# Kernel optimization log

Hardware: AMD Instinct MI355X
Metric: run time of the kernel (lower is better)

The kernel has to match this reference:

```python
import jax, jax.numpy as jnp
import numpy as np

N_HEADS, D_MODEL, D_HEAD = 16, 1024, 64
INIT_STD = 0.02


def setup_inputs() -> dict:
    key = jax.random.key(0)
    ks = jax.random.split(key, 5)
    x = jax.random.normal(ks[0], (4, 2048, D_MODEL), dtype=jnp.float32)
    W_Q = jax.random.normal(ks[1], (N_HEADS, D_MODEL, D_HEAD), dtype=jnp.float32) * INIT_STD
    W_K = jax.random.normal(ks[2], (N_HEADS, D_MODEL, D_HEAD), dtype=jnp.float32) * INIT_STD
    W_V = jax.random.normal(ks[3], (N_HEADS, D_MODEL, D_HEAD), dtype=jnp.float32) * INIT_STD
    W_O = jax.random.normal(ks[4], (N_HEADS, D_HEAD, D_MODEL), dtype=jnp.float32) * INIT_STD
    b_Q = jnp.zeros((N_HEADS, D_HEAD), dtype=jnp.float32)
    b_K = jnp.zeros((N_HEADS, D_HEAD), dtype=jnp.float32)
    b_V = jnp.zeros((N_HEADS, D_HEAD), dtype=jnp.float32)
    b_O = jnp.zeros((D_MODEL,), dtype=jnp.float32)
    return {"normalized_resid_pre": x, "W_Q": W_Q, "W_K": W_K, "W_V": W_V,
            "W_O": W_O, "b_Q": b_Q, "b_K": b_K, "b_V": b_V, "b_O": b_O}


def reference(normalized_resid_pre, W_Q, W_K, W_V, W_O, b_Q, b_K, b_V, b_O):
    x = normalized_resid_pre  # [b, s, d_model]
    q = jnp.einsum('bsm,hmd->bshd', x, W_Q) + b_Q  # [b, s, h, d_head]
    k = jnp.einsum('bsm,hmd->bshd', x, W_K) + b_K
    v = jnp.einsum('bsm,hmd->bshd', x, W_V) + b_V
    scores = jnp.einsum('bqhd,bkhd->bhqk', q, k) / jnp.sqrt(jnp.float32(D_HEAD))
    S = x.shape[1]
    causal = jnp.tril(jnp.ones((S, S), dtype=bool))  # keep key_pos <= query_pos
    scores = jnp.where(causal, scores, jnp.finfo(scores.dtype).min)
    pattern = jax.nn.softmax(scores, axis=-1)  # [b, h, q, k]
    z = jnp.einsum('bhqk,bkhd->bqhd', pattern, v)
    attn_out = jnp.einsum('bqhd,hdm->bqm', z, W_O) + b_O
    return attn_out
```

## Files before the change

kernel.cpp:

```cpp
#include <hip/hip_runtime.h>
#include <hip/hip_bf16.h>
#include <math.h>

typedef __bf16 bf16_t;
typedef bf16_t bf16x8 __attribute__((ext_vector_type(8)));
typedef float f32x4 __attribute__((ext_vector_type(4)));

#define BB 4
#define SS 2048
#define HH 16
#define DMODEL 1024
#define DHEAD 64

#define QSCALE 0.18033688011112042f

__device__ inline unsigned short f2bf(float f) {
    union { __hip_bfloat16 h; unsigned short u; } cvt;
    cvt.h = __float2bfloat16(f);
    return cvt.u;
}

__device__ __forceinline__ void gll16(const unsigned short* g, unsigned short* l) {
    __builtin_amdgcn_global_load_lds(
        (const __attribute__((address_space(1))) unsigned int*)(g),
        (__attribute__((address_space(3))) unsigned int*)(l), 16, 0, 0);
}


__global__ void pack_x(const float* __restrict__ x, unsigned short* __restrict__ xb) {
    int i = blockIdx.x * 256 + threadIdx.x;
    const float4 v = ((const float4*)x)[i];
    unsigned short o[4] = { f2bf(v.x), f2bf(v.y), f2bf(v.z), f2bf(v.w) };
    *(uint2*)(xb + 4 * (size_t)i) = *(uint2*)o;
}

__global__ void pack_wqkv(const float* __restrict__ wq, const float* __restrict__ wk,
                          const float* __restrict__ wv, unsigned short* __restrict__ out) {
    int idx = blockIdx.x * 256 + threadIdx.x;
    int k  = idx & 1023;
    int n  = idx >> 10;
    int mat = n >> 10;
    int n1 = n & 1023;
    int h = n1 >> 6, d = n1 & 63;
    const float* w = (mat == 0) ? wq : (mat == 1) ? wk : wv;
    out[idx] = f2bf(w[(h << 16) + (k << 6) + d]);
}

__global__ void pack_wo(const float* __restrict__ wo, unsigned short* __restrict__ out) {
    int idx = blockIdx.x * 256 + threadIdx.x;
    int k = idx & 1023, n = idx >> 10;
    out[idx] = f2bf(wo[(k << 10) + n]);
}


__global__ __launch_bounds__(256) void gemm_qkv(
    const unsigned short* __restrict__ xb,
    const unsigned short* __restrict__ wT,
    const float* __restrict__ bq, const float* __restrict__ bk, const float* __restrict__ bv,
    unsigned short* __restrict__ qws, unsigned short* __restrict__ kws,
    unsigned short* __restrict__ vtw)
{
    __shared__ __align__(16) unsigned short lA[128 * 32];
    __shared__ __align__(16) unsigned short lB[128 * 32];
    const int t = threadIdx.x;
    const int lane = t & 63;
    const int w = t >> 6;
    const int quad = lane >> 4;
    const int l15 = lane & 15;
    const int n0 = blockIdx.x * 128;
    const int m0 = blockIdx.y * 128;
    const int wm = (w >> 1) * 64;
    const int wn = (w & 1) * 64;
    const int mat = n0 >> 10;

    f32x4 acc[4][4] = {};

    const int srow = w * 16 + (lane >> 2);
    const int scol = (lane & 3) * 8;
    const unsigned short* Ag0 = xb + (size_t)(m0 + srow) * 1024 + scol;
    const unsigned short* Ag1 = Ag0 + (size_t)64 * 1024;
    const unsigned short* Bg0 = wT + (size_t)(n0 + srow) * 1024 + scol;
    const unsigned short* Bg1 = Bg0 + (size_t)64 * 1024;
    unsigned short* lA0 = lA + (w * 16) * 32;
    unsigned short* lA1 = lA + (64 + w * 16) * 32;
    unsigned short* lB0 = lB + (w * 16) * 32;
    unsigned short* lB1 = lB + (64 + w * 16) * 32;

    if (mat != 2) {
        for (int kt = 0; kt < 1024; kt += 32) {
            __syncthreads();
            gll16(Ag0 + kt, lA0);
            gll16(Ag1 + kt, lA1);
            gll16(Bg0 + kt, lB0);
            gll16(Bg1 + kt, lB1);
            __syncthreads();
            bf16x8 af[4], bfr[4];
#pragma unroll
            for (int i = 0; i < 4; i++) {
                af[i]  = *(const bf16x8*)(lA + (wm + i * 16 + l15) * 32 + quad * 8);
                bfr[i] = *(const bf16x8*)(lB + (wn + i * 16 + l15) * 32 + quad * 8);
            }
#pragma unroll
            for (int i = 0; i < 4; i++)
#pragma unroll
                for (int j = 0; j < 4; j++)
                    acc[i][j] = __builtin_amdgcn_mfma_f32_16x16x32_bf16(bfr[j], af[i], acc[i][j], 0, 0, 0);
        }
        const int b = m0 >> 11;
        const float* bias_p = (mat == 0) ? bq : bk;
        const float scale = (mat == 0) ? QSCALE : 1.0f;
        unsigned short* dst = (mat == 0) ? qws : kws;
#pragma unroll
        for (int j = 0; j < 4; j++) {
            const int noff = wn + j * 16 + quad * 4;
            const int h = noff >> 6;
            const int hglob = ((n0 & 1023) >> 6) + h;
            const int dbase = noff & 63;
            const float4 bv4 = *(const float4*)(bias_p + hglob * 64 + dbase);
            const float bias_r[4] = { bv4.x, bv4.y, bv4.z, bv4.w };
#pragma unroll
            for (int i = 0; i < 4; i++) {
                const int s = (m0 & 2047) + wm + i * 16 + l15;
                unsigned short pk[4];
#pragma unroll
                for (int r = 0; r < 4; r++) pk[r] = f2bf((acc[i][j][r] + bias_r[r]) * scale);
                *(uint2*)(dst + (size_t)((b * 16 + hglob) * 2048 + s) * 64 + dbase) = *(uint2*)pk;
            }
        }
    } else {
        for (int kt = 0; kt < 1024; kt += 32) {
            __syncthreads();
            gll16(Ag0 + kt, lA0);
            gll16(Ag1 + kt, lA1);
            gll16(Bg0 + kt, lB0);
            gll16(Bg1 + kt, lB1);
            __syncthreads();
            bf16x8 af[4], bfr[4];
#pragma unroll
            for (int i = 0; i < 4; i++) {
                af[i]  = *(const bf16x8*)(lA + (wm + i * 16 + l15) * 32 + quad * 8);
                bfr[i] = *(const bf16x8*)(lB + (wn + i * 16 + l15) * 32 + quad * 8);
            }
#pragma unroll
            for (int i = 0; i < 4; i++)
#pragma unroll
                for (int j = 0; j < 4; j++)
                    acc[i][j] = __builtin_amdgcn_mfma_f32_16x16x32_bf16(af[i], bfr[j], acc[i][j], 0, 0, 0);
        }
        const int b = m0 >> 11;
#pragma unroll
        for (int j = 0; j < 4; j++) {
            const int n1 = (n0 & 1023) + wn + j * 16 + l15;
            const int h = n1 >> 6, d = n1 & 63;
            const float bias = bv[h * 64 + d];
#pragma unroll
            for (int i = 0; i < 4; i++) {
                const int s0 = (m0 & 2047) + wm + i * 16 + quad * 4;
                unsigned short pk[4];
#pragma unroll
                for (int r = 0; r < 4; r++) pk[r] = f2bf(acc[i][j][r] + bias);
                *(uint2*)(vtw + ((size_t)(b * 16 + h) * 64 + d) * 2048 + s0) = *(uint2*)pk;
            }
        }
    }
}


__global__ __launch_bounds__(256) void attn3(
    const unsigned short* __restrict__ qws,
    const unsigned short* __restrict__ kws,
    const unsigned short* __restrict__ vtw,
    unsigned short* __restrict__ zb)
{
    __shared__ __align__(16) unsigned short Ks[64 * 64];
    __shared__ __align__(16) unsigned short Vs[64 * 64];
    __shared__ __align__(16) unsigned short Ps[4 * 16 * 64];

    const int t = threadIdx.x;
    const int lane = t & 63;
    const int w = t >> 6;
    const int quad = lane >> 4;
    const int l15 = lane & 15;
    const int hi = l15 >> 3;
    const int lo = l15 & 7;

    const int qt = 31 - (blockIdx.x >> 6);
    const int bh = blockIdx.x & 63;
    const int q0 = qt * 64;
    const int qbase = q0 + w * 16;
    const size_t base = (size_t)bh * SS * DHEAD;
    const unsigned short* Q = qws + base;
    const unsigned short* K = kws + base;
    const unsigned short* Vt = vtw + base;

    bf16x8 qf0 = *(const bf16x8*)(Q + (size_t)(qbase + l15) * 64 + quad * 8);
    bf16x8 qf1 = *(const bf16x8*)(Q + (size_t)(qbase + l15) * 64 + 32 + quad * 8);

    f32x4 o[4] = {};
    float lsum[4] = {0.f, 0.f, 0.f, 0.f};
    unsigned short* Pw = Ps + w * 16 * 64;

    const int sr = t >> 2;
    const int g0 = t & 3;
    const int sw0 = ((g0 ^ (sr & 7)) << 3);
    const int sw1 = (((g0 + 4) ^ (sr & 7)) << 3);
    unsigned short* ksw = Ks + sr * 64;
    unsigned short* vsw = Vs + sr * 64;
    const unsigned short* Kg = K + (size_t)sr * 64 + g0 * 8;
    const unsigned short* Vg = Vt + (size_t)sr * 2048 + g0 * 8;

    const int gq0 = ((quad ^ lo) << 3);
    const int gq1 = (((quad + 4) ^ lo) << 3);

    const int nch = qt + 1;

    uint4 kr0 = *(const uint4*)(Kg);
    uint4 kr1 = *(const uint4*)(Kg + 32);
    uint4 vr0 = *(const uint4*)(Vg);
    uint4 vr1 = *(const uint4*)(Vg + 32);

    for (int c = 0; c < nch; c++) {
        __builtin_amdgcn_sched_barrier(0);
        __builtin_amdgcn_s_barrier();
        *(uint4*)(ksw + sw0) = kr0;
        *(uint4*)(ksw + sw1) = kr1;
        *(uint4*)(vsw + sw0) = vr0;
        *(uint4*)(vsw + sw1) = vr1;
        if (c + 1 < nch) {
            const unsigned short* kp = Kg + (size_t)(c + 1) * 64 * 64;
            const unsigned short* vp = Vg + (size_t)(c + 1) * 64;
            kr0 = *(const uint4*)(kp);
            kr1 = *(const uint4*)(kp + 32);
            vr0 = *(const uint4*)(vp);
            vr1 = *(const uint4*)(vp + 32);
        }
        asm volatile("s_waitcnt lgkmcnt(0)" ::: "memory");
        __builtin_amdgcn_s_barrier();
        __builtin_amdgcn_sched_barrier(0);

        f32x4 s[4];
        __builtin_amdgcn_s_setprio(1);
#pragma unroll
        for (int sub = 0; sub < 4; sub++) {
            const unsigned short* kr = Ks + (sub * 16 + l15) * 64;
            bf16x8 kf0 = *(const bf16x8*)(kr + gq0);
            bf16x8 kf1 = *(const bf16x8*)(kr + gq1);
            f32x4 sv = {};
            sv = __builtin_amdgcn_mfma_f32_16x16x32_bf16(qf0, kf0, sv, 0, 0, 0);
            sv = __builtin_amdgcn_mfma_f32_16x16x32_bf16(qf1, kf1, sv, 0, 0, 0);
            s[sub] = sv;
        }
        __builtin_amdgcn_s_setprio(0);

        const int kb = c * 64;
        if (c == nch - 1) {
            const int qg = qbase + quad * 4;
#pragma unroll
            for (int sub = 0; sub < 4; sub++) {
                const int key = kb + sub * 16 + l15;
#pragma unroll
                for (int r = 0; r < 4; r++) {
                    float p = (key > qg + r) ? 0.f : exp2f(s[sub][r]);
                    lsum[r] += p;
                    const int q = quad * 4 + r;
                    Pw[q * 64 + (((sub * 2 + hi) ^ (q & 7)) << 3) + lo] = f2bf(p);
                }
            }
        } else {
#pragma unroll
            for (int sub = 0; sub < 4; sub++)
#pragma unroll
                for (int r = 0; r < 4; r++) {
                    float p = exp2f(s[sub][r]);
                    lsum[r] += p;
                    const int q = quad * 4 + r;
                    Pw[q * 64 + (((sub * 2 + hi) ^ (q & 7)) << 3) + lo] = f2bf(p);
                }
        }
        asm volatile("s_waitcnt lgkmcnt(0)" ::: "memory");
        bf16x8 pf0 = *(const bf16x8*)(Pw + l15 * 64 + gq0);
        bf16x8 pf1 = *(const bf16x8*)(Pw + l15 * 64 + gq1);
        __builtin_amdgcn_s_setprio(1);
#pragma unroll
        for (int dt = 0; dt < 4; dt++) {
            const unsigned short* vrp = Vs + (dt * 16 + l15) * 64;
            bf16x8 vf0 = *(const bf16x8*)(vrp + gq0);
            bf16x8 vf1 = *(const bf16x8*)(vrp + gq1);
            o[dt] = __builtin_amdgcn_mfma_f32_16x16x32_bf16(vf0, pf0, o[dt], 0, 0, 0);
            o[dt] = __builtin_amdgcn_mfma_f32_16x16x32_bf16(vf1, pf1, o[dt], 0, 0, 0);
        }
        __builtin_amdgcn_s_setprio(0);
    }

#pragma unroll
    for (int r = 0; r < 4; r++) {
        float v = lsum[r];
        v += __shfl_xor(v, 1);
        v += __shfl_xor(v, 2);
        v += __shfl_xor(v, 4);
        v += __shfl_xor(v, 8);
        lsum[r] = v;
    }
    const int srcl = (l15 >> 2) << 4;
    float t0 = __shfl(lsum[0], srcl);
    float t1 = __shfl(lsum[1], srcl);
    float t2 = __shfl(lsum[2], srcl);
    float t3 = __shfl(lsum[3], srcl);
    const int rr = l15 & 3;
    float den = (rr == 0) ? t0 : (rr == 1) ? t1 : (rr == 2) ? t2 : t3;
    const float inv = 1.0f / den;

    const int b = bh >> 4, h = bh & 15;
    const int q = qbase + l15;
    unsigned short* zrow = zb + (size_t)(b * 2048 + q) * 1024 + h * 64 + quad * 4;
#pragma unroll
    for (int dt = 0; dt < 4; dt++) {
        unsigned short pk[4];
#pragma unroll
        for (int r = 0; r < 4; r++) pk[r] = f2bf(o[dt][r] * inv);
        *(uint2*)(zrow + dt * 16) = *(uint2*)pk;
    }
}


__global__ __launch_bounds__(256) void gemm_out(
    const unsigned short* __restrict__ zb,
    const unsigned short* __restrict__ wT,
    const float* __restrict__ bo,
    float* __restrict__ out)
{
    __shared__ __align__(16) unsigned short lA[128 * 32];
    __shared__ __align__(16) unsigned short lB[128 * 32];
    const int t = threadIdx.x;
    const int lane = t & 63;
    const int w = t >> 6;
    const int quad = lane >> 4;
    const int l15 = lane & 15;
    const int n0 = blockIdx.x * 128;
    const int m0 = blockIdx.y * 128;
    const int wm = (w >> 1) * 64;
    const int wn = (w & 1) * 64;

    f32x4 acc[4][4] = {};

    const int srow = w * 16 + (lane >> 2);
    const int scol = (lane & 3) * 8;
    const unsigned short* Ag0 = zb + (size_t)(m0 + srow) * 1024 + scol;
    const unsigned short* Ag1 = Ag0 + (size_t)64 * 1024;
    const unsigned short* Bg0 = wT + (size_t)(n0 + srow) * 1024 + scol;
    const unsigned short* Bg1 = Bg0 + (size_t)64 * 1024;
    unsigned short* lA0 = lA + (w * 16) * 32;
    unsigned short* lA1 = lA + (64 + w * 16) * 32;
    unsigned short* lB0 = lB + (w * 16) * 32;
    unsigned short* lB1 = lB + (64 + w * 16) * 32;

    for (int kt = 0; kt < 1024; kt += 32) {
        __syncthreads();
        gll16(Ag0 + kt, lA0);
        gll16(Ag1 + kt, lA1);
        gll16(Bg0 + kt, lB0);
        gll16(Bg1 + kt, lB1);
        __syncthreads();
        bf16x8 af[4], bfr[4];
#pragma unroll
        for (int i = 0; i < 4; i++) {
            af[i]  = *(const bf16x8*)(lA + (wm + i * 16 + l15) * 32 + quad * 8);
            bfr[i] = *(const bf16x8*)(lB + (wn + i * 16 + l15) * 32 + quad * 8);
        }
#pragma unroll
        for (int i = 0; i < 4; i++)
#pragma unroll
            for (int j = 0; j < 4; j++)
                acc[i][j] = __builtin_amdgcn_mfma_f32_16x16x32_bf16(bfr[j], af[i], acc[i][j], 0, 0, 0);
    }

#pragma unroll
    for (int j = 0; j < 4; j++) {
        const int nbase = n0 + wn + j * 16 + quad * 4;
        const float4 bv4 = *(const float4*)(bo + nbase);
#pragma unroll
        for (int i = 0; i < 4; i++) {
            const int s = m0 + wm + i * 16 + l15;
            float4 v;
            v.x = acc[i][j][0] + bv4.x;
            v.y = acc[i][j][1] + bv4.y;
            v.z = acc[i][j][2] + bv4.z;
            v.w = acc[i][j][3] + bv4.w;
            *(float4*)(out + (size_t)s * 1024 + nbase) = v;
        }
    }
}


extern "C" void kernel_launch(void* const* d_in, const int* in_sizes, int n_in,
                              void* d_out, int out_size, void* d_ws, size_t ws_size,
                              hipStream_t stream) {
    const float* x  = (const float*)d_in[0];
    const float* WQ = (const float*)d_in[1];
    const float* WK = (const float*)d_in[2];
    const float* WV = (const float*)d_in[3];
    const float* WO = (const float*)d_in[4];
    const float* bQ = (const float*)d_in[5];
    const float* bK = (const float*)d_in[6];
    const float* bV = (const float*)d_in[7];
    const float* bO = (const float*)d_in[8];
    float* out = (float*)d_out;

    char* ws = (char*)d_ws;
    unsigned short* xb   = (unsigned short*)ws;
    unsigned short* wqkv = (unsigned short*)(ws + (16u << 20));
    unsigned short* woT  = (unsigned short*)(ws + (22u << 20));
    unsigned short* qws  = (unsigned short*)(ws + (24u << 20));
    unsigned short* kws  = (unsigned short*)(ws + (40u << 20));
    unsigned short* vtw  = (unsigned short*)(ws + (56u << 20));
    unsigned short* zbuf = xb;

    pack_x<<<8192, 256, 0, stream>>>(x, xb);
    pack_wqkv<<<(3072 * 1024) / 256, 256, 0, stream>>>(WQ, WK, WV, wqkv);
    pack_wo<<<(1024 * 1024) / 256, 256, 0, stream>>>(WO, woT);
    gemm_qkv<<<dim3(24, 64), 256, 0, stream>>>(xb, wqkv, bQ, bK, bV, qws, kws, vtw);
    attn3<<<2048, 256, 0, stream>>>(qws, kws, vtw, zbuf);
    gemm_out<<<dim3(8, 64), 256, 0, stream>>>(zbuf, woT, bO, out);
}
```

Measured before the change: 303.3 us.

## Rewrite QKV GEMM as 256x256 tile, 8-wave double-buffered pipelined kernel

Replaces the 128x128, 4-wave QKV projection GEMM with a 256x256 tile, 8-wave kernel. It double-buffers LDS with BK=64 and XOR-swizzled layout, and interleaves global-to-LDS staging with four MFMA phases per k-step using barriers, sched_barrier and setprio. The aim is to raise data reuse per loaded byte, hide global load latency behind MFMA work, and cut LDS bank conflicts. In exchange it uses much more LDS and registers (acc[8][4]) and launches a smaller grid of 384 blocks, which can hurt occupancy and wave balance across CUs.

```diff
diff --git a/kernel.cpp b/kernel.cpp
--- a/kernel.cpp
+++ b/kernel.cpp
@@ -53,112 +53,208 @@
 }
 
 
-__global__ __launch_bounds__(256) void gemm_qkv(
+template <bool SWAP>
+__device__ __forceinline__ void mf16(f32x4& d, bf16x8 a, bf16x8 b) {
+    if constexpr (SWAP)
+        d = __builtin_amdgcn_mfma_f32_16x16x32_bf16(b, a, d, 0, 0, 0);
+    else
+        d = __builtin_amdgcn_mfma_f32_16x16x32_bf16(a, b, d, 0, 0, 0);
+}
+
+#define GBAR()   __builtin_amdgcn_s_barrier()
+#define SCHEDB() __builtin_amdgcn_sched_barrier(0)
+#define WLGKM0() asm volatile("s_waitcnt lgkmcnt(0)" ::: "memory")
+
+template <bool SWAP>
+__device__ __forceinline__ void kloop256(
+    unsigned short (*sAb)[256][64], unsigned short (*sBb)[256][64],
+    const unsigned short* gA0, const unsigned short* gA1,
+    const unsigned short* gB0, const unsigned short* gB1,
+    int w, int wr, int wc, int l15, int quad, int lo,
+    f32x4 (&acc)[8][4])
+{
+    auto STAGE = [&](const unsigned short* g, unsigned short* lb, int T) {
+        const unsigned short* s = g + T * 64;
+        gll16(s, lb + w * 8 * 64);
+        gll16(s + 64 * 1024, lb + (64 + w * 8) * 64);
+    };
+
+    STAGE(gB0, &sBb[0][0][0],   0);
+    STAGE(gA0, &sAb[0][0][0],   0);
+    STAGE(gB1, &sBb[0][128][0], 0);
+    STAGE(gA1, &sAb[0][128][0], 0);
+    STAGE(gB0, &sBb[1][0][0],   1);
+    STAGE(gA0, &sAb[1][0][0],   1);
+    asm volatile("s_waitcnt vmcnt(4)" ::: "memory");
+    GBAR();
+
+#pragma unroll 2
+    for (int kt = 0; kt < 16; ++kt) {
+        const int bsel = kt & 1;
+        unsigned short (*A)[64] = sAb[bsel];
+        unsigned short (*B)[64] = sBb[bsel];
+        bf16x8 a0[4][2], a1[4][2], bA[2][2], bB[2][2];
+
+#pragma unroll
+        for (int mi = 0; mi < 4; mi++) {
+            a0[mi][0] = *(const bf16x8*)&A[wr * 128 + mi * 16 + l15][(quad ^ lo) * 8];
+            a0[mi][1] = *(const bf16x8*)&A[wr * 128 + mi * 16 + l15][((4 | quad) ^ lo) * 8];
+        }
+#pragma unroll
+        for (int nj = 0; nj < 2; nj++) {
+            bA[nj][0] = *(const bf16x8*)&B[wc * 64 + nj * 16 + l15][(quad ^ lo) * 8];
+            bA[nj][1] = *(const bf16x8*)&B[wc * 64 + nj * 16 + l15][((4 | quad) ^ lo) * 8];
+        }
+        if (kt + 1 < 16) STAGE(gB1, &sBb[(kt + 1) & 1][128][0], kt + 1);
+        GBAR();
+        WLGKM0();
+        SCHEDB();
+        __builtin_amdgcn_s_setprio(1);
+#pragma unroll
+        for (int mi = 0; mi < 4; mi++)
+#pragma unroll
+            for (int nj = 0; nj < 2; nj++) {
+                mf16<SWAP>(acc[mi][nj], a0[mi][0], bA[nj][0]);
+                mf16<SWAP>(acc[mi][nj], a0[mi][1], bA[nj][1]);
+            }
+        __builtin_amdgcn_s_setprio(0);
+        SCHEDB();
+        GBAR();
+
+#pragma unroll
+        for (int nj = 0; nj < 2; nj++) {
+            bB[nj][0] = *(const bf16x8*)&B[wc * 64 + (nj + 2) * 16 + l15][(quad ^ lo) * 8];
+            bB[nj][1] = *(const bf16x8*)&B[wc * 64 + (nj + 2) * 16 + l15][((4 | quad) ^ lo) * 8];
+        }
+        if (kt + 1 < 16) STAGE(gA1, &sAb[(kt + 1) & 1][128][0], kt + 1);
+        GBAR();
+        WLGKM0();
+        SCHEDB();
+        __builtin_amdgcn_s_setprio(1);
+#pragma unroll
+        for (int mi = 0; mi < 4; mi++)
+#pragma unroll
+            for (int nj = 0; nj < 2; nj++) {
+                mf16<SWAP>(acc[mi][nj + 2], a0[mi][0], bB[nj][0]);
+                mf16<SWAP>(acc[mi][nj + 2], a0[mi][1], bB[nj][1]);
+            }
+        __builtin_amdgcn_s_setprio(0);
+        SCHEDB();
+        GBAR();
+
+#pragma unroll
+        for (int mi = 0; mi < 4; mi++) {
+            a1[mi][0] = *(const bf16x8*)&A[wr * 128 + 64 + mi * 16 + l15][(quad ^ lo) * 8];
+            a1[mi][1] = *(const bf16x8*)&A[wr * 128 + 64 + mi * 16 + l15][((4 | quad) ^ lo) * 8];
+        }
+        if (kt + 2 < 16) STAGE(gB0, &sBb[kt & 1][0][0], kt + 2);
+        GBAR();
+        WLGKM0();
+        SCHEDB();
+        __builtin_amdgcn_s_setprio(1);
+#pragma unroll
+        for (int mi = 0; mi < 4; mi++)
+#pragma unroll
+            for (int nj = 0; nj < 2; nj++) {
+                mf16<SWAP>(acc[4 + mi][nj + 2], a1[mi][0], bB[nj][0]);
+                mf16<SWAP>(acc[4 + mi][nj + 2], a1[mi][1], bB[nj][1]);
+            }
+        __builtin_amdgcn_s_setprio(0);
+        SCHEDB();
+        GBAR();
+
+        if (kt + 2 < 16) STAGE(gA0, &sAb[kt & 1][0][0], kt + 2);
+        GBAR();
+        WLGKM0();
+        SCHEDB();
+        __builtin_amdgcn_s_setprio(1);
+#pragma unroll
+        for (int mi = 0; mi < 4; mi++)
+#pragma unroll
+            for (int nj = 0; nj < 2; nj++) {
+                mf16<SWAP>(acc[4 + mi][nj], a1[mi][0], bA[nj][0]);
+                mf16<SWAP>(acc[4 + mi][nj], a1[mi][1], bA[nj][1]);
+            }
+        __builtin_amdgcn_s_setprio(0);
+        SCHEDB();
+        if (kt == 14) {
+            asm volatile("s_waitcnt vmcnt(0)" ::: "memory");
+        } else if (kt < 14) {
+            asm volatile("s_waitcnt vmcnt(4)" ::: "memory");
+        }
+        GBAR();
+    }
+}
+
+__global__ __launch_bounds__(512, 2) void gemm_qkv8(
     const unsigned short* __restrict__ xb,
     const unsigned short* __restrict__ wT,
     const float* __restrict__ bq, const float* __restrict__ bk, const float* __restrict__ bv,
     unsigned short* __restrict__ qws, unsigned short* __restrict__ kws,
     unsigned short* __restrict__ vtw)
 {
-    __shared__ __align__(16) unsigned short lA[128 * 32];
-    __shared__ __align__(16) unsigned short lB[128 * 32];
+    __shared__ __align__(16) unsigned short sA[2][256][64];
+    __shared__ __align__(16) unsigned short sB[2][256][64];
+
     const int t = threadIdx.x;
     const int lane = t & 63;
     const int w = t >> 6;
     const int quad = lane >> 4;
     const int l15 = lane & 15;
-    const int n0 = blockIdx.x * 128;
-    const int m0 = blockIdx.y * 128;
-    const int wm = (w >> 1) * 64;
-    const int wn = (w & 1) * 64;
+    const int lo = l15 & 7;
+    const int wr = w >> 2;
+    const int wc = w & 3;
+    const int n0 = blockIdx.x * 256;
+    const int m0 = blockIdx.y * 256;
     const int mat = n0 >> 10;
 
-    f32x4 acc[4][4] = {};
-
-    const int srow = w * 16 + (lane >> 2);
-    const int scol = (lane & 3) * 8;
-    const unsigned short* Ag0 = xb + (size_t)(m0 + srow) * 1024 + scol;
-    const unsigned short* Ag1 = Ag0 + (size_t)64 * 1024;
-    const unsigned short* Bg0 = wT + (size_t)(n0 + srow) * 1024 + scol;
-    const unsigned short* Bg1 = Bg0 + (size_t)64 * 1024;
-    unsigned short* lA0 = lA + (w * 16) * 32;
-    unsigned short* lA1 = lA + (64 + w * 16) * 32;
-    unsigned short* lB0 = lB + (w * 16) * 32;
-    unsigned short* lB1 = lB + (64 + w * 16) * 32;
+    const int sr8 = lane >> 3;
+    const size_t soff = (size_t)(w * 8 + sr8) * 1024 + (size_t)(((lane & 7) ^ sr8) * 8);
+    const unsigned short* gA0 = xb + (size_t)m0 * 1024 + soff;
+    const unsigned short* gA1 = xb + (size_t)(m0 + 128) * 1024 + soff;
+    const unsigned short* gB0 = wT + (size_t)n0 * 1024 + soff;
+    const unsigned short* gB1 = wT + (size_t)(n0 + 128) * 1024 + soff;
+
+    f32x4 acc[8][4] = {};
+
+    const int b = m0 >> 11;
+    const int m0r = m0 & 2047;
 
     if (mat != 2) {
-        for (int kt = 0; kt < 1024; kt += 32) {
-            __syncthreads();
-            gll16(Ag0 + kt, lA0);
-            gll16(Ag1 + kt, lA1);
-            gll16(Bg0 + kt, lB0);
-            gll16(Bg1 + kt, lB1);
-            __syncthreads();
-            bf16x8 af[4], bfr[4];
-#pragma unroll
-            for (int i = 0; i < 4; i++) {
-                af[i]  = *(const bf16x8*)(lA + (wm + i * 16 + l15) * 32 + quad * 8);
-                bfr[i] = *(const bf16x8*)(lB + (wn + i * 16 + l15) * 32 + quad * 8);
-            }
-#pragma unroll
-            for (int i = 0; i < 4; i++)
-#pragma unroll
-                for (int j = 0; j < 4; j++)
-                    acc[i][j] = __builtin_amdgcn_mfma_f32_16x16x32_bf16(bfr[j], af[i], acc[i][j], 0, 0, 0);
-        }
-        const int b = m0 >> 11;
+        kloop256<true>(sA, sB, gA0, gA1, gB0, gB1, w, wr, wc, l15, quad, lo, acc);
         const float* bias_p = (mat == 0) ? bq : bk;
         const float scale = (mat == 0) ? QSCALE : 1.0f;
         unsigned short* dst = (mat == 0) ? qws : kws;
 #pragma unroll
-        for (int j = 0; j < 4; j++) {
-            const int noff = wn + j * 16 + quad * 4;
-            const int h = noff >> 6;
-            const int hglob = ((n0 & 1023) >> 6) + h;
-            const int dbase = noff & 63;
-            const float4 bv4 = *(const float4*)(bias_p + hglob * 64 + dbase);
+        for (int nj = 0; nj < 4; nj++) {
+            const int noff = wc * 64 + nj * 16 + quad * 4;
+            const int nmat = (n0 & 1023) + noff;
+            const int h = nmat >> 6;
+            const int dbase = nmat & 63;
+            const float4 bv4 = *(const float4*)(bias_p + h * 64 + dbase);
             const float bias_r[4] = { bv4.x, bv4.y, bv4.z, bv4.w };
 #pragma unroll
-            for (int i = 0; i < 4; i++) {
-                const int s = (m0 & 2047) + wm + i * 16 + l15;
+            for (int mig = 0; mig < 8; mig++) {
+                const int s = m0r + wr * 128 + mig * 16 + l15;
                 unsigned short pk[4];
 #pragma unroll
-                for (int r = 0; r < 4; r++) pk[r] = f2bf((acc[i][j][r] + bias_r[r]) * scale);
-                *(uint2*)(dst + (size_t)((b * 16 + hglob) * 2048 + s) * 64 + dbase) = *(uint2*)pk;
+                for (int r = 0; r < 4; r++) pk[r] = f2bf((acc[mig][nj][r] + bias_r[r]) * scale);
+                *(uint2*)(dst + (size_t)((b * 16 + h) * 2048 + s) * 64 + dbase) = *(uint2*)pk;
             }
         }
     } else {
-        for (int kt = 0; kt < 1024; kt += 32) {
-            __syncthreads();
-            gll16(Ag0 + kt, lA0);
-            gll16(Ag1 + kt, lA1);
-            gll16(Bg0 + kt, lB0);
-            gll16(Bg1 + kt, lB1);
-            __syncthreads();
-            bf16x8 af[4], bfr[4];
-#pragma unroll
-            for (int i = 0; i < 4; i++) {
-                af[i]  = *(const bf16x8*)(lA + (wm + i * 16 + l15) * 32 + quad * 8);
-                bfr[i] = *(const bf16x8*)(lB + (wn + i * 16 + l15) * 32 + quad * 8);
-            }
-#pragma unroll
-            for (int i = 0; i < 4; i++)
-#pragma unroll
-                for (int j = 0; j < 4; j++)
-                    acc[i][j] = __builtin_amdgcn_mfma_f32_16x16x32_bf16(af[i], bfr[j], acc[i][j], 0, 0, 0);
-        }
-        const int b = m0 >> 11;
-#pragma unroll
-        for (int j = 0; j < 4; j++) {
-            const int n1 = (n0 & 1023) + wn + j * 16 + l15;
+        kloop256<false>(sA, sB, gA0, gA1, gB0, gB1, w, wr, wc, l15, quad, lo, acc);
+#pragma unroll
+        for (int nj = 0; nj < 4; nj++) {
+            const int n1 = (n0 & 1023) + wc * 64 + nj * 16 + l15;
             const int h = n1 >> 6, d = n1 & 63;
             const float bias = bv[h * 64 + d];
 #pragma unroll
-            for (int i = 0; i < 4; i++) {
-                const int s0 = (m0 & 2047) + wm + i * 16 + quad * 4;
+            for (int mig = 0; mig < 8; mig++) {
+                const int s0 = m0r + wr * 128 + mig * 16 + quad * 4;
                 unsigned short pk[4];
 #pragma unroll
-                for (int r = 0; r < 4; r++) pk[r] = f2bf(acc[i][j][r] + bias);
+                for (int r = 0; r < 4; r++) pk[r] = f2bf(acc[mig][nj][r] + bias);
                 *(uint2*)(vtw + ((size_t)(b * 16 + h) * 64 + d) * 2048 + s0) = *(uint2*)pk;
             }
         }
@@ -418,7 +514,7 @@
     pack_x<<<8192, 256, 0, stream>>>(x, xb);
     pack_wqkv<<<(3072 * 1024) / 256, 256, 0, stream>>>(WQ, WK, WV, wqkv);
     pack_wo<<<(1024 * 1024) / 256, 256, 0, stream>>>(WO, woT);
-    gemm_qkv<<<dim3(24, 64), 256, 0, stream>>>(xb, wqkv, bQ, bK, bV, qws, kws, vtw);
+    gemm_qkv8<<<dim3(12, 32), 512, 0, stream>>>(xb, wqkv, bQ, bK, bV, qws, kws, vtw);
     attn3<<<2048, 256, 0, stream>>>(qws, kws, vtw, zbuf);
     gemm_out<<<dim3(8, 64), 256, 0, stream>>>(zbuf, woT, bO, out);
 }
```

After: 306.2 us. No clear change (+0.9%).

## Double-buffer K/V tiles in attention, transpose score MFMA, merge pack kernels

Applied to the files above, without the earlier changes.

The attention kernel now keeps two LDS buffers for K and V. The next chunk is written while the current one is computed, which removes one of the two block barriers per chunk. Operands of the score MFMA are swapped, so each lane holds one query row. That makes the row-sum reduction a two-step shuffle and lets P be written as packed 8-byte stores instead of scalar ones. The three bf16 packing kernels are merged into one launch to cut launch overhead. The cost is extra LDS (double-buffered tiles), which may lower occupancy.

```diff
diff --git a/kernel.cpp b/kernel.cpp
--- a/kernel.cpp
+++ b/kernel.cpp
@@ -27,29 +27,31 @@
 }
 
 
-__global__ void pack_x(const float* __restrict__ x, unsigned short* __restrict__ xb) {
-    int i = blockIdx.x * 256 + threadIdx.x;
-    const float4 v = ((const float4*)x)[i];
-    unsigned short o[4] = { f2bf(v.x), f2bf(v.y), f2bf(v.z), f2bf(v.w) };
-    *(uint2*)(xb + 4 * (size_t)i) = *(uint2*)o;
-}
-
-__global__ void pack_wqkv(const float* __restrict__ wq, const float* __restrict__ wk,
-                          const float* __restrict__ wv, unsigned short* __restrict__ out) {
-    int idx = blockIdx.x * 256 + threadIdx.x;
-    int k  = idx & 1023;
-    int n  = idx >> 10;
-    int mat = n >> 10;
-    int n1 = n & 1023;
-    int h = n1 >> 6, d = n1 & 63;
-    const float* w = (mat == 0) ? wq : (mat == 1) ? wk : wv;
-    out[idx] = f2bf(w[(h << 16) + (k << 6) + d]);
-}
-
-__global__ void pack_wo(const float* __restrict__ wo, unsigned short* __restrict__ out) {
-    int idx = blockIdx.x * 256 + threadIdx.x;
-    int k = idx & 1023, n = idx >> 10;
-    out[idx] = f2bf(wo[(k << 10) + n]);
+__global__ void pack_all(const float* __restrict__ x,
+                         const float* __restrict__ wq, const float* __restrict__ wk,
+                         const float* __restrict__ wv, const float* __restrict__ wo,
+                         unsigned short* __restrict__ xb, unsigned short* __restrict__ wqkv,
+                         unsigned short* __restrict__ woT) {
+    const int bid = blockIdx.x;
+    if (bid < 8192) {
+        int i = bid * 256 + threadIdx.x;
+        const float4 v = ((const float4*)x)[i];
+        unsigned short o[4] = { f2bf(v.x), f2bf(v.y), f2bf(v.z), f2bf(v.w) };
+        *(uint2*)(xb + 4 * (size_t)i) = *(uint2*)o;
+    } else if (bid < 8192 + 12288) {
+        int idx = (bid - 8192) * 256 + threadIdx.x;
+        int k  = idx & 1023;
+        int n  = idx >> 10;
+        int mat = n >> 10;
+        int n1 = n & 1023;
+        int h = n1 >> 6, d = n1 & 63;
+        const float* wsrc = (mat == 0) ? wq : (mat == 1) ? wk : wv;
+        wqkv[idx] = f2bf(wsrc[(h << 16) + (k << 6) + d]);
+    } else {
+        int idx = (bid - 20480) * 256 + threadIdx.x;
+        int k = idx & 1023, n = idx >> 10;
+        woT[idx] = f2bf(wo[(k << 10) + n]);
+    }
 }
 
 
@@ -166,163 +168,6 @@
 }
 
 
-__global__ __launch_bounds__(256) void attn3(
-    const unsigned short* __restrict__ qws,
-    const unsigned short* __restrict__ kws,
-    const unsigned short* __restrict__ vtw,
-    unsigned short* __restrict__ zb)
-{
-    __shared__ __align__(16) unsigned short Ks[64 * 64];
-    __shared__ __align__(16) unsigned short Vs[64 * 64];
-    __shared__ __align__(16) unsigned short Ps[4 * 16 * 64];
-
-    const int t = threadIdx.x;
-    const int lane = t & 63;
-    const int w = t >> 6;
-    const int quad = lane >> 4;
-    const int l15 = lane & 15;
-    const int hi = l15 >> 3;
-    const int lo = l15 & 7;
-
-    const int qt = 31 - (blockIdx.x >> 6);
-    const int bh = blockIdx.x & 63;
-    const int q0 = qt * 64;
-    const int qbase = q0 + w * 16;
-    const size_t base = (size_t)bh * SS * DHEAD;
-    const unsigned short* Q = qws + base;
-    const unsigned short* K = kws + base;
-    const unsigned short* Vt = vtw + base;
-
-    bf16x8 qf0 = *(const bf16x8*)(Q + (size_t)(qbase + l15) * 64 + quad * 8);
-    bf16x8 qf1 = *(const bf16x8*)(Q + (size_t)(qbase + l15) * 64 + 32 + quad * 8);
-
-    f32x4 o[4] = {};
-    float lsum[4] = {0.f, 0.f, 0.f, 0.f};
-    unsigned short* Pw = Ps + w * 16 * 64;
-
-    const int sr = t >> 2;
-    const int g0 = t & 3;
-    const int sw0 = ((g0 ^ (sr & 7)) << 3);
-    const int sw1 = (((g0 + 4) ^ (sr & 7)) << 3);
-    unsigned short* ksw = Ks + sr * 64;
-    unsigned short* vsw = Vs + sr * 64;
-    const unsigned short* Kg = K + (size_t)sr * 64 + g0 * 8;
-    const unsigned short* Vg = Vt + (size_t)sr * 2048 + g0 * 8;
-
-    const int gq0 = ((quad ^ lo) << 3);
-    const int gq1 = (((quad + 4) ^ lo) << 3);
-
-    const int nch = qt + 1;
-
-    uint4 kr0 = *(const uint4*)(Kg);
-    uint4 kr1 = *(const uint4*)(Kg + 32);
-    uint4 vr0 = *(const uint4*)(Vg);
-    uint4 vr1 = *(const uint4*)(Vg + 32);
-
-    for (int c = 0; c < nch; c++) {
-        __builtin_amdgcn_sched_barrier(0);
-        __builtin_amdgcn_s_barrier();
-        *(uint4*)(ksw + sw0) = kr0;
-        *(uint4*)(ksw + sw1) = kr1;
-        *(uint4*)(vsw + sw0) = vr0;
-        *(uint4*)(vsw + sw1) = vr1;
-        if (c + 1 < nch) {
-            const unsigned short* kp = Kg + (size_t)(c + 1) * 64 * 64;
-            const unsigned short* vp = Vg + (size_t)(c + 1) * 64;
-            kr0 = *(const uint4*)(kp);
-            kr1 = *(const uint4*)(kp + 32);
-            vr0 = *(const uint4*)(vp);
-            vr1 = *(const uint4*)(vp + 32);
-        }
-        asm volatile("s_waitcnt lgkmcnt(0)" ::: "memory");
-        __builtin_amdgcn_s_barrier();
-        __builtin_amdgcn_sched_barrier(0);
-
-        f32x4 s[4];
-        __builtin_amdgcn_s_setprio(1);
-#pragma unroll
-        for (int sub = 0; sub < 4; sub++) {
-            const unsigned short* kr = Ks + (sub * 16 + l15) * 64;
-            bf16x8 kf0 = *(const bf16x8*)(kr + gq0);
-            bf16x8 kf1 = *(const bf16x8*)(kr + gq1);
-            f32x4 sv = {};
-            sv = __builtin_amdgcn_mfma_f32_16x16x32_bf16(qf0, kf0, sv, 0, 0, 0);
-            sv = __builtin_amdgcn_mfma_f32_16x16x32_bf16(qf1, kf1, sv, 0, 0, 0);
-            s[sub] = sv;
-        }
-        __builtin_amdgcn_s_setprio(0);
-
-        const int kb = c * 64;
-        if (c == nch - 1) {
-            const int qg = qbase + quad * 4;
-#pragma unroll
-            for (int sub = 0; sub < 4; sub++) {
-                const int key = kb + sub * 16 + l15;
-#pragma unroll
-                for (int r = 0; r < 4; r++) {
-                    float p = (key > qg + r) ? 0.f : exp2f(s[sub][r]);
-                    lsum[r] += p;
-                    const int q = quad * 4 + r;
-                    Pw[q * 64 + (((sub * 2 + hi) ^ (q & 7)) << 3) + lo] = f2bf(p);
-                }
-            }
-        } else {
-#pragma unroll
-            for (int sub = 0; sub < 4; sub++)
-#pragma unroll
-                for (int r = 0; r < 4; r++) {
-                    float p = exp2f(s[sub][r]);
-                    lsum[r] += p;
-                    const int q = quad * 4 + r;
-                    Pw[q * 64 + (((sub * 2 + hi) ^ (q & 7)) << 3) + lo] = f2bf(p);
-                }
-        }
-        asm volatile("s_waitcnt lgkmcnt(0)" ::: "memory");
-        bf16x8 pf0 = *(const bf16x8*)(Pw + l15 * 64 + gq0);
-        bf16x8 pf1 = *(const bf16x8*)(Pw + l15 * 64 + gq1);
-        __builtin_amdgcn_s_setprio(1);
-#pragma unroll
-        for (int dt = 0; dt < 4; dt++) {
-            const unsigned short* vrp = Vs + (dt * 16 + l15) * 64;
-            bf16x8 vf0 = *(const bf16x8*)(vrp + gq0);
-            bf16x8 vf1 = *(const bf16x8*)(vrp + gq1);
-            o[dt] = __builtin_amdgcn_mfma_f32_16x16x32_bf16(vf0, pf0, o[dt], 0, 0, 0);
-            o[dt] = __builtin_amdgcn_mfma_f32_16x16x32_bf16(vf1, pf1, o[dt], 0, 0, 0);
-        }
-        __builtin_amdgcn_s_setprio(0);
-    }
-
-#pragma unroll
-    for (int r = 0; r < 4; r++) {
-        float v = lsum[r];
-        v += __shfl_xor(v, 1);
-        v += __shfl_xor(v, 2);
-        v += __shfl_xor(v, 4);
-        v += __shfl_xor(v, 8);
-        lsum[r] = v;
-    }
-    const int srcl = (l15 >> 2) << 4;
-    float t0 = __shfl(lsum[0], srcl);
-    float t1 = __shfl(lsum[1], srcl);
-    float t2 = __shfl(lsum[2], srcl);
-    float t3 = __shfl(lsum[3], srcl);
-    const int rr = l15 & 3;
-    float den = (rr == 0) ? t0 : (rr == 1) ? t1 : (rr == 2) ? t2 : t3;
-    const float inv = 1.0f / den;
-
-    const int b = bh >> 4, h = bh & 15;
-    const int q = qbase + l15;
-    unsigned short* zrow = zb + (size_t)(b * 2048 + q) * 1024 + h * 64 + quad * 4;
-#pragma unroll
-    for (int dt = 0; dt < 4; dt++) {
-        unsigned short pk[4];
-#pragma unroll
-        for (int r = 0; r < 4; r++) pk[r] = f2bf(o[dt][r] * inv);
-        *(uint2*)(zrow + dt * 16) = *(uint2*)pk;
-    }
-}
-
-
 __global__ __launch_bounds__(256) void gemm_out(
     const unsigned short* __restrict__ zb,
     const unsigned short* __restrict__ wT,
@@ -392,6 +237,202 @@
 }
 
 
+__device__ __forceinline__ f32x4 mfma_bf16(bf16x8 a, bf16x8 b, f32x4 c) {
+    return __builtin_amdgcn_mfma_f32_16x16x32_bf16(a, b, c, 0, 0, 0);
+}
+
+__device__ __forceinline__ void attn_chunk(
+    int c, int nch, int qbase, bool last,
+    const unsigned short* Kg, const unsigned short* Vg,
+    unsigned short* curK, unsigned short* curV,
+    unsigned short* nxtK, unsigned short* nxtV,
+    uint4& kin0, uint4& kin1, uint4& vin0, uint4& vin1,
+    uint4& kout0, uint4& kout1, uint4& vout0, uint4& vout1,
+    unsigned short* Pw,
+    unsigned short* pws0, unsigned short* pws1, unsigned short* pws2, unsigned short* pws3,
+    int sr, int sw0, int sw1, int l15, int quad, int gq0, int gq1,
+    bf16x8 qf0, bf16x8 qf1, f32x4 (&o)[4], float& lsum)
+{
+    if (c + 1 < nch) {
+        *(uint4*)(nxtK + sr * 64 + sw0) = kin0;
+        *(uint4*)(nxtK + sr * 64 + sw1) = kin1;
+        *(uint4*)(nxtV + sr * 64 + sw0) = vin0;
+        *(uint4*)(nxtV + sr * 64 + sw1) = vin1;
+    }
+    if (c + 2 < nch) {
+        const unsigned short* kp = Kg + (size_t)(c + 2) * 64 * 64;
+        const unsigned short* vp = Vg + (size_t)(c + 2) * 64;
+        kout0 = *(const uint4*)(kp);
+        kout1 = *(const uint4*)(kp + 32);
+        vout0 = *(const uint4*)(vp);
+        vout1 = *(const uint4*)(vp + 32);
+    }
+
+    f32x4 s[4];
+    __builtin_amdgcn_s_setprio(1);
+#pragma unroll
+    for (int sub = 0; sub < 4; sub++) {
+        const unsigned short* kr = curK + (sub * 16 + l15) * 64;
+        bf16x8 kf0 = *(const bf16x8*)(kr + gq0);
+        bf16x8 kf1 = *(const bf16x8*)(kr + gq1);
+        f32x4 sv = {};
+        sv = mfma_bf16(kf0, qf0, sv);
+        sv = mfma_bf16(kf1, qf1, sv);
+        s[sub] = sv;
+    }
+    __builtin_amdgcn_s_setprio(0);
+
+    const int kb = c * 64;
+    if (last) {
+        const int qg = qbase + l15;
+#pragma unroll
+        for (int sub = 0; sub < 4; sub++) {
+            const int k0 = kb + sub * 16 + quad * 4;
+            unsigned short pk[4];
+#pragma unroll
+            for (int r = 0; r < 4; r++) {
+                float p = (k0 + r > qg) ? 0.f : exp2f(s[sub][r]);
+                lsum += p;
+                pk[r] = f2bf(p);
+            }
+            unsigned short* wp = (sub == 0) ? pws0 : (sub == 1) ? pws1 : (sub == 2) ? pws2 : pws3;
+            *(uint2*)wp = *(uint2*)pk;
+        }
+    } else {
+#pragma unroll
+        for (int sub = 0; sub < 4; sub++) {
+            unsigned short pk[4];
+#pragma unroll
+            for (int r = 0; r < 4; r++) {
+                float p = exp2f(s[sub][r]);
+                lsum += p;
+                pk[r] = f2bf(p);
+            }
+            unsigned short* wp = (sub == 0) ? pws0 : (sub == 1) ? pws1 : (sub == 2) ? pws2 : pws3;
+            *(uint2*)wp = *(uint2*)pk;
+        }
+    }
+    asm volatile("s_waitcnt lgkmcnt(0)" ::: "memory");
+    bf16x8 pf0 = *(const bf16x8*)(Pw + l15 * 64 + gq0);
+    bf16x8 pf1 = *(const bf16x8*)(Pw + l15 * 64 + gq1);
+    __builtin_amdgcn_s_setprio(1);
+#pragma unroll
+    for (int dt = 0; dt < 4; dt++) {
+        const unsigned short* vrp = curV + (dt * 16 + l15) * 64;
+        bf16x8 vf0 = *(const bf16x8*)(vrp + gq0);
+        bf16x8 vf1 = *(const bf16x8*)(vrp + gq1);
+        o[dt] = mfma_bf16(vf0, pf0, o[dt]);
+        o[dt] = mfma_bf16(vf1, pf1, o[dt]);
+    }
+    __builtin_amdgcn_s_setprio(0);
+    __builtin_amdgcn_s_barrier();
+    __builtin_amdgcn_sched_barrier(0);
+}
+
+__global__ __launch_bounds__(256) void attn3(
+    const unsigned short* __restrict__ qws,
+    const unsigned short* __restrict__ kws,
+    const unsigned short* __restrict__ vtw,
+    unsigned short* __restrict__ zb)
+{
+    __shared__ __align__(16) unsigned short Ks0[64 * 64];
+    __shared__ __align__(16) unsigned short Ks1[64 * 64];
+    __shared__ __align__(16) unsigned short Vs0[64 * 64];
+    __shared__ __align__(16) unsigned short Vs1[64 * 64];
+    __shared__ __align__(16) unsigned short Ps[4 * 16 * 64];
+
+    const int t = threadIdx.x;
+    const int lane = t & 63;
+    const int w = t >> 6;
+    const int quad = lane >> 4;
+    const int l15 = lane & 15;
+    const int lo = l15 & 7;
+
+    const int qt = 31 - (blockIdx.x >> 6);
+    const int bh = blockIdx.x & 63;
+    const int q0 = qt * 64;
+    const int qbase = q0 + w * 16;
+    const size_t base = (size_t)bh * SS * DHEAD;
+    const unsigned short* Q = qws + base;
+    const unsigned short* K = kws + base;
+    const unsigned short* Vt = vtw + base;
+
+    bf16x8 qf0 = *(const bf16x8*)(Q + (size_t)(qbase + l15) * 64 + quad * 8);
+    bf16x8 qf1 = *(const bf16x8*)(Q + (size_t)(qbase + l15) * 64 + 32 + quad * 8);
+
+    f32x4 o[4] = {};
+    float lsum = 0.f;
+    unsigned short* Pw = Ps + w * 16 * 64;
+
+    const int sr = t >> 2;
+    const int g0 = t & 3;
+    const int sw0 = ((g0 ^ (sr & 7)) << 3);
+    const int sw1 = (((g0 + 4) ^ (sr & 7)) << 3);
+    const unsigned short* Kg = K + (size_t)sr * 64 + g0 * 8;
+    const unsigned short* Vg = Vt + (size_t)sr * 2048 + g0 * 8;
+
+    const int gq0 = ((quad ^ lo) << 3);
+    const int gq1 = (((quad + 4) ^ lo) << 3);
+
+    unsigned short* pwr = Pw + l15 * 64;
+    unsigned short* pws0 = pwr + (((0 + quad) ^ (lo << 1)) << 2);
+    unsigned short* pws1 = pwr + (((4 + quad) ^ (lo << 1)) << 2);
+    unsigned short* pws2 = pwr + (((8 + quad) ^ (lo << 1)) << 2);
+    unsigned short* pws3 = pwr + (((12 + quad) ^ (lo << 1)) << 2);
+
+    const int nch = qt + 1;
+
+    uint4 ka0 = *(const uint4*)(Kg);
+    uint4 ka1 = *(const uint4*)(Kg + 32);
+    uint4 va0 = *(const uint4*)(Vg);
+    uint4 va1 = *(const uint4*)(Vg + 32);
+    *(uint4*)(Ks0 + sr * 64 + sw0) = ka0;
+    *(uint4*)(Ks0 + sr * 64 + sw1) = ka1;
+    *(uint4*)(Vs0 + sr * 64 + sw0) = va0;
+    *(uint4*)(Vs0 + sr * 64 + sw1) = va1;
+    uint4 kb0 = {}, kb1 = {}, vb0 = {}, vb1 = {};
+    if (nch > 1) {
+        kb0 = *(const uint4*)(Kg + 64 * 64);
+        kb1 = *(const uint4*)(Kg + 64 * 64 + 32);
+        vb0 = *(const uint4*)(Vg + 64);
+        vb1 = *(const uint4*)(Vg + 64 + 32);
+    }
+    asm volatile("s_waitcnt lgkmcnt(0)" ::: "memory");
+    __builtin_amdgcn_s_barrier();
+    __builtin_amdgcn_sched_barrier(0);
+
+    for (int c = 0; c < nch; c += 2) {
+        attn_chunk(c, nch, qbase, c == nch - 1, Kg, Vg,
+                   Ks0, Vs0, Ks1, Vs1,
+                   kb0, kb1, vb0, vb1, ka0, ka1, va0, va1,
+                   Pw, pws0, pws1, pws2, pws3,
+                   sr, sw0, sw1, l15, quad, gq0, gq1, qf0, qf1, o, lsum);
+        if (c + 1 < nch)
+            attn_chunk(c + 1, nch, qbase, c + 1 == nch - 1, Kg, Vg,
+                       Ks1, Vs1, Ks0, Vs0,
+                       ka0, ka1, va0, va1, kb0, kb1, vb0, vb1,
+                       Pw, pws0, pws1, pws2, pws3,
+                       sr, sw0, sw1, l15, quad, gq0, gq1, qf0, qf1, o, lsum);
+    }
+
+    float v = lsum;
+    v += __shfl_xor(v, 16);
+    v += __shfl_xor(v, 32);
+    const float inv = 1.0f / v;
+
+    const int b = bh >> 4, h = bh & 15;
+    const int q = qbase + l15;
+    unsigned short* zrow = zb + (size_t)(b * 2048 + q) * 1024 + h * 64 + quad * 4;
+#pragma unroll
+    for (int dt = 0; dt < 4; dt++) {
+        unsigned short pk[4];
+#pragma unroll
+        for (int r = 0; r < 4; r++) pk[r] = f2bf(o[dt][r] * inv);
+        *(uint2*)(zrow + dt * 16) = *(uint2*)pk;
+    }
+}
+
+
 extern "C" void kernel_launch(void* const* d_in, const int* in_sizes, int n_in,
                               void* d_out, int out_size, void* d_ws, size_t ws_size,
                               hipStream_t stream) {
@@ -415,9 +456,7 @@
     unsigned short* vtw  = (unsigned short*)(ws + (56u << 20));
     unsigned short* zbuf = xb;
 
-    pack_x<<<8192, 256, 0, stream>>>(x, xb);
-    pack_wqkv<<<(3072 * 1024) / 256, 256, 0, stream>>>(WQ, WK, WV, wqkv);
-    pack_wo<<<(1024 * 1024) / 256, 256, 0, stream>>>(WO, woT);
+    pack_all<<<24576, 256, 0, stream>>>(x, WQ, WK, WV, WO, xb, wqkv, woT);
     gemm_qkv<<<dim3(24, 64), 256, 0, stream>>>(xb, wqkv, bQ, bK, bV, qws, kws, vtw);
     attn3<<<2048, 256, 0, stream>>>(qws, kws, vtw, zbuf);
     gemm_out<<<dim3(8, 64), 256, 0, stream>>>(zbuf, woT, bO, out);
```

New measurement: 299.9 us. No clear change (-1.1%).
